# Optimization experiments

Measured on AMD Instinct MI355X. Metric: run time of the kernel, lower is better.

## Reference

```python
import jax, jax.numpy as jnp
import numpy as np

N_GENE, N_DIS = 100_000, 50_000   # node counts per node type
D = 128                            # hidden_channels (= input dim, required by skipsum)
E = 800_000                        # edges per edge type
L = 2                              # num_layers
EPS = 1e-12                        # torch F.normalize eps


def setup_inputs() -> dict:
    key = jax.random.key(0)
    ks = jax.random.split(key, 9)
    s = 1.0 / np.sqrt(D)
    return {
        "x_gene": jax.random.normal(ks[0], (N_GENE, D), jnp.float32),
        "x_disease": jax.random.normal(ks[1], (N_DIS, D), jnp.float32),
        # per (layer, edge_type) SAGEConv weights: lin_l (neighbors), lin_r (root), bias
        # edge_type 0: gene->disease, edge_type 1: disease->gene
        "Wl": jax.random.normal(ks[2], (L, 2, D, D), jnp.float32) * s,
        "Wr": jax.random.normal(ks[3], (L, 2, D, D), jnp.float32) * s,
        "b": jax.random.normal(ks[4], (L, 2, D), jnp.float32) * 0.01,
        "src_g2d": jax.random.randint(ks[5], (E,), 0, N_GENE, dtype=jnp.int32),
        "dst_g2d": jax.random.randint(ks[6], (E,), 0, N_DIS, dtype=jnp.int32),
        "src_d2g": jax.random.randint(ks[7], (E,), 0, N_DIS, dtype=jnp.int32),
        "dst_d2g": jax.random.randint(ks[8], (E,), 0, N_GENE, dtype=jnp.int32),
    }


def _sage(x_src, x_dst, src, dst, Wl, Wr, b, n_dst):
    # SAGEConv with aggr='mean': lin_l(mean_{j in N(i)} x_j) + lin_r(x_i) + bias
    msg = jnp.take(x_src, src, axis=0)                                   # [E, D] gather
    summed = jax.ops.segment_sum(msg, dst, num_segments=n_dst)           # [n_dst, D]
    cnt = jax.ops.segment_sum(jnp.ones_like(src, dtype=x_src.dtype), dst,
                              num_segments=n_dst)                        # [n_dst]
    mean = summed / jnp.maximum(cnt, 1.0)[:, None]                       # isolated nodes -> 0
    return mean @ Wl.T + x_dst @ Wr.T + b


def _l2norm(x):
    n = jnp.linalg.norm(x, axis=-1, keepdims=True)
    return x / jnp.maximum(n, EPS)


def reference(x_gene, x_disease, Wl, Wr, b, src_g2d, dst_g2d, src_d2g, dst_d2g):
    xg, xd = x_gene, x_disease
    for i in range(L):
        # to_hetero: one conv per edge type; macro_aggregation='sum' across edge types
        # (each dst type here receives exactly one edge type)
        hd = _sage(xg, xd, src_g2d, dst_g2d, Wl[i, 0], Wr[i, 0], b[i, 0], N_DIS)
        hg = _sage(xd, xg, src_d2g, dst_d2g, Wl[i, 1], Wr[i, 1], b[i, 1], N_GENE)
        if i < L - 1:  # hidden layers get the activation
            hg, hd = jax.nn.relu(hg), jax.nn.relu(hd)
        # L2_norm=True -> normalize every layer
        hg, hd = _l2norm(hg), _l2norm(hd)
        # skipsum
        xg, xd = hg + xg, hd + xd
    return xg, xd
```

## Files before the change

kernel.cpp:

```cpp
#include <hip/hip_runtime.h>
#include <math.h>

#define NG 100000
#define ND 50000
#define NTOT 150000
#define DIM 128
#define NE 800000
#define EPSN 1e-12f

#define RPB 256
#define NBT_D2 196
#define NBT_G2 391

#define NBK 586
#define SCB 128
#define EPB 12500

typedef __bf16 bf16x8 __attribute__((ext_vector_type(8)));
typedef float f32x4 __attribute__((ext_vector_type(4)));
typedef unsigned int uint32;

__device__ __forceinline__ ushort rne_bf16(float f) {
  uint32 u = __builtin_bit_cast(uint32, f);
  u += 0x7fffu + ((u >> 16) & 1u);
  return (ushort)(u >> 16);
}


__global__ void zero_ints(int* __restrict__ p, int n) {
  int i = blockIdx.x * 256 + threadIdx.x;
  if (i < n) p[i] = 0;
}

__global__ void bucket_count(const int* __restrict__ dst_g2d, const int* __restrict__ dst_d2g,
                             int* __restrict__ bcnt) {
  __shared__ int h[NBK];
  for (int j = threadIdx.x; j < NBK; j += 256) h[j] = 0;
  __syncthreads();
  int stride = gridDim.x * 256;
  for (int i = blockIdx.x * 256 + threadIdx.x; i < 2 * NE; i += stride) {
    int d = (i < NE) ? dst_g2d[i] : ND + dst_d2g[i - NE];
    atomicAdd(&h[d >> 8], 1);
  }
  __syncthreads();
  for (int j = threadIdx.x; j < NBK; j += 256)
    if (h[j]) atomicAdd(&bcnt[j], h[j]);
}

__global__ void bucket_scan(const int* __restrict__ bcnt, int* __restrict__ bbase,
                            int* __restrict__ bcur) {
  __shared__ int s[1024];
  int t = threadIdx.x;
  s[t] = (t < NBK) ? bcnt[t] : 0;
  __syncthreads();
  for (int off = 1; off < 1024; off <<= 1) {
    int v = (t >= off) ? s[t - off] : 0;
    __syncthreads();
    s[t] += v;
    __syncthreads();
  }
  if (t < NBK) {
    int e = (t > 0) ? s[t - 1] : 0;
    bbase[t] = e;
    bcur[t] = e;
  }
  if (t == 0) bbase[NBK] = 2 * NE;
}

__global__ void bucket_scatter(const int* __restrict__ src_g2d, const int* __restrict__ dst_g2d,
                               const int* __restrict__ src_d2g, const int* __restrict__ dst_d2g,
                               int* __restrict__ bcur, int2* __restrict__ pairs) {
  __shared__ int h[NBK];
  __shared__ int base[NBK];
  int e0 = blockIdx.x * EPB;
  int e1 = e0 + EPB;
  if (e1 > 2 * NE) e1 = 2 * NE;
  for (int j = threadIdx.x; j < NBK; j += 256) h[j] = 0;
  __syncthreads();
  for (int i = e0 + threadIdx.x; i < e1; i += 256) {
    int d = (i < NE) ? dst_g2d[i] : ND + dst_d2g[i - NE];
    atomicAdd(&h[d >> 8], 1);
  }
  __syncthreads();
  for (int j = threadIdx.x; j < NBK; j += 256) {
    int c = h[j];
    base[j] = c ? atomicAdd(&bcur[j], c) : 0;
    h[j] = 0;
  }
  __syncthreads();
  for (int i = e0 + threadIdx.x; i < e1; i += 256) {
    int d, s;
    if (i < NE) {
      d = dst_g2d[i];
      s = src_g2d[i];
    } else {
      d = ND + dst_d2g[i - NE];
      s = src_d2g[i - NE];
    }
    int bkt = d >> 8;
    int p = base[bkt] + atomicAdd(&h[bkt], 1);
    pairs[p] = make_int2(d, s);
  }
}

__global__ void bucket_to_csr(const int* __restrict__ bbase, const int2* __restrict__ pairs,
                              int* __restrict__ off, int* __restrict__ csr) {
  __shared__ int cnt[256];
  __shared__ int ss[256];
  int b = blockIdx.x, t = threadIdx.x;
  int n0 = b << 8;
  int s0 = bbase[b], s1 = bbase[b + 1];
  cnt[t] = 0;
  __syncthreads();
  for (int i = s0 + t; i < s1; i += 256) atomicAdd(&cnt[pairs[i].x - n0], 1);
  __syncthreads();
  int x = cnt[t];
  ss[t] = x;
  __syncthreads();
  for (int o = 1; o < 256; o <<= 1) {
    int y = (t >= o) ? ss[t - o] : 0;
    __syncthreads();
    ss[t] += y;
    __syncthreads();
  }
  int abs0 = s0 + ss[t] - x;
  int node = n0 + t;
  if (node < NTOT) off[node] = abs0;
  if (node == NTOT - 1) off[NTOT] = 2 * NE;
  __syncthreads();
  cnt[t] = abs0;
  __syncthreads();
  for (int i = s0 + t; i < s1; i += 256) {
    int2 e = pairs[i];
    int p = atomicAdd(&cnt[e.x - n0], 1);
    csr[p] = e.y;
  }
}


__global__ void to_bf16_all(const float* __restrict__ xg, const float* __restrict__ xd,
                            ushort* __restrict__ yg, ushort* __restrict__ yd) {
  int i = blockIdx.x * 256 + threadIdx.x;
  if (i >= NTOT * 16) return;
  const float* x;
  ushort* y;
  int j;
  if (i < NG * 16) {
    x = xg; y = yg; j = i;
  } else {
    x = xd; y = yd; j = i - NG * 16;
  }
  const float4* px = (const float4*)x;
  float4 a = px[2 * j], b = px[2 * j + 1];
  float v[8] = {a.x, a.y, a.z, a.w, b.x, b.y, b.z, b.w};
  uint32 u[4];
#pragma unroll
  for (int k = 0; k < 4; k++)
    u[k] = (uint32)rne_bf16(v[2 * k]) | ((uint32)rne_bf16(v[2 * k + 1]) << 16);
  ((int4*)y)[j] = make_int4((int)u[0], (int)u[1], (int)u[2], (int)u[3]);
}


__global__ void split_w(const float* __restrict__ Wl, const float* __restrict__ Wr,
                        ushort* __restrict__ WlH, ushort* __restrict__ WlL,
                        ushort* __restrict__ WrH, ushort* __restrict__ WrL) {
  int i = blockIdx.x * 256 + threadIdx.x;
  if (i >= 4 * 128 * 128) return;
  {
    float a = Wl[i];
    uint32 u = __builtin_bit_cast(uint32, a);
    float hf = __builtin_bit_cast(float, u & 0xffff0000u);
    WlH[i] = (ushort)(u >> 16);
    WlL[i] = (ushort)(__builtin_bit_cast(uint32, a - hf) >> 16);
  }
  {
    float a = Wr[i];
    uint32 u = __builtin_bit_cast(uint32, a);
    float hf = __builtin_bit_cast(float, u & 0xffff0000u);
    WrH[i] = (ushort)(u >> 16);
    WrL[i] = (ushort)(__builtin_bit_cast(uint32, a - hf) >> 16);
  }
}


__device__ __forceinline__ void acc8(float* a, int4 u) {
  uint32 w;
  w = (uint32)u.x;
  a[0] += __builtin_bit_cast(float, w << 16);
  a[1] += __builtin_bit_cast(float, w & 0xffff0000u);
  w = (uint32)u.y;
  a[2] += __builtin_bit_cast(float, w << 16);
  a[3] += __builtin_bit_cast(float, w & 0xffff0000u);
  w = (uint32)u.z;
  a[4] += __builtin_bit_cast(float, w << 16);
  a[5] += __builtin_bit_cast(float, w & 0xffff0000u);
  w = (uint32)u.w;
  a[6] += __builtin_bit_cast(float, w << 16);
  a[7] += __builtin_bit_cast(float, w & 0xffff0000u);
}

__global__ void agg_comb(const ushort* __restrict__ xg_bf, const ushort* __restrict__ xd_bf,
                         const int* __restrict__ off, const int* __restrict__ csr,
                         ushort* __restrict__ agg_bf) {
  int node = (blockIdx.x * 256 + threadIdx.x) >> 4;
  if (node >= NTOT) return;
  int l16 = threadIdx.x & 15;
  const int4* xs = (const int4*)((node < ND) ? xg_bf : xd_bf);
  int e0 = off[node], e1 = off[node + 1];
  float a[8] = {0.f, 0.f, 0.f, 0.f, 0.f, 0.f, 0.f, 0.f};
  int e = e0;
  for (; e + 3 < e1; e += 4) {
    int s0 = csr[e], s1 = csr[e + 1], s2 = csr[e + 2], s3 = csr[e + 3];
    int4 v0 = xs[(size_t)s0 * 16 + l16];
    int4 v1 = xs[(size_t)s1 * 16 + l16];
    int4 v2 = xs[(size_t)s2 * 16 + l16];
    int4 v3 = xs[(size_t)s3 * 16 + l16];
    acc8(a, v0);
    acc8(a, v1);
    acc8(a, v2);
    acc8(a, v3);
  }
  for (; e + 1 < e1; e += 2) {
    int s0 = csr[e], s1 = csr[e + 1];
    int4 v0 = xs[(size_t)s0 * 16 + l16];
    int4 v1 = xs[(size_t)s1 * 16 + l16];
    acc8(a, v0);
    acc8(a, v1);
  }
  if (e < e1) acc8(a, xs[(size_t)csr[e] * 16 + l16]);
  int deg = e1 - e0;
  float inv = (deg > 0) ? 1.f / (float)deg : 0.f;
  uint32 u[4];
#pragma unroll
  for (int j = 0; j < 4; j++)
    u[j] = (uint32)rne_bf16(a[2 * j] * inv) | ((uint32)rne_bf16(a[2 * j + 1] * inv) << 16);
  *(int4*)&agg_bf[(size_t)node * DIM + l16 * 8] =
      make_int4((int)u[0], (int)u[1], (int)u[2], (int)u[3]);
}


__device__ __forceinline__ void split8(const float* xp, bf16x8& hi, bf16x8& lo) {
  float4 f0 = *(const float4*)xp;
  float4 f1 = *(const float4*)(xp + 4);
  float v[8] = {f0.x, f0.y, f0.z, f0.w, f1.x, f1.y, f1.z, f1.w};
  uint32 hw[4], lw[4];
#pragma unroll
  for (int j = 0; j < 4; j++) {
    uint32 u0 = __builtin_bit_cast(uint32, v[2 * j]);
    uint32 u1 = __builtin_bit_cast(uint32, v[2 * j + 1]);
    float hf0 = __builtin_bit_cast(float, u0 & 0xffff0000u);
    float hf1 = __builtin_bit_cast(float, u1 & 0xffff0000u);
    uint32 l0 = __builtin_bit_cast(uint32, v[2 * j] - hf0) >> 16;
    uint32 l1 = __builtin_bit_cast(uint32, v[2 * j + 1] - hf1) >> 16;
    hw[j] = (u0 >> 16) | ((u1 >> 16) << 16);
    lw[j] = l0 | (l1 << 16);
  }
  hi = __builtin_bit_cast(bf16x8, make_int4((int)hw[0], (int)hw[1], (int)hw[2], (int)hw[3]));
  lo = __builtin_bit_cast(bf16x8, make_int4((int)lw[0], (int)lw[1], (int)lw[2], (int)lw[3]));
}

__launch_bounds__(256, 2)
__global__ void sage_dual(const ushort* __restrict__ agg_bf, const float* __restrict__ xd,
                          const float* __restrict__ xg, const ushort* __restrict__ WlH,
                          const ushort* __restrict__ WlL, const ushort* __restrict__ WrH,
                          const ushort* __restrict__ WrL, const float* __restrict__ bias_all,
                          float* __restrict__ outd, float* __restrict__ outg,
                          ushort* __restrict__ xbf_d, ushort* __restrict__ xbf_g, int layer,
                          int relu, int write_bf) {
  __shared__ __align__(16) char smem[65536];

  int b = blockIdx.x;
  const float* X;
  float* O;
  ushort* OBF;
  int n, set, r0g, cbase;
  if (b < NBT_D2) {
    X = xd; O = outd; OBF = xbf_d; n = ND; set = layer * 2; r0g = b * RPB; cbase = 0;
  } else {
    X = xg; O = outg; OBF = xbf_g; n = NG; set = layer * 2 + 1;
    r0g = (b - NBT_D2) * RPB; cbase = ND;
  }
  const ushort* Wplanes[4] = {WlH + set * 16384, WlL + set * 16384, WrH + set * 16384,
                              WrL + set * 16384};
  const float* bias = bias_all + set * 128;

  int tid = threadIdx.x;
  int wave = tid >> 6, lane = tid & 63;
  int m = lane & 15, q = lane >> 4;

  auto stageW = [&](const ushort* Ph, const ushort* Pl) {
#pragma unroll
    for (int i = 0; i < 16; i++) {
      int c = tid + i * 256;
      int p = c >> 11;
      int Bl = (c & 2047) * 16;
      const ushort* src = p ? Pl : Ph;
      int4 v = *(const int4*)((const char*)src + Bl);
      int dst = p * 32768 + (Bl ^ (((Bl >> 8) & 7) << 4));
      *(int4*)(smem + dst) = v;
    }
  };

  f32x4 acc[4][8];
#pragma unroll
  for (int mt = 0; mt < 4; mt++)
#pragma unroll
    for (int nt = 0; nt < 8; nt++) acc[mt][nt] = (f32x4)0.f;

  int rb = r0g + wave * 64;

  stageW(Wplanes[0], Wplanes[1]);
  __syncthreads();
#pragma unroll
  for (int ks = 0; ks < 4; ks++) {
    int kc = ks * 32 + q * 8;
    int kb = ks * 64 + q * 16;
    bf16x8 a[4];
#pragma unroll
    for (int mt = 0; mt < 4; mt++) {
      int r = rb + mt * 16 + m;
      if (r >= n) r = n - 1;
      a[mt] = __builtin_bit_cast(bf16x8, *(const int4*)&agg_bf[(size_t)(cbase + r) * DIM + kc]);
    }
#pragma unroll
    for (int nt = 0; nt < 8; nt++) {
      int nn = nt * 16 + m;
      int wb = (nn * 256 + kb) ^ ((nn & 7) << 4);
      bf16x8 bh = *(const bf16x8*)(smem + wb);
      bf16x8 bl = *(const bf16x8*)(smem + 32768 + wb);
#pragma unroll
      for (int mt = 0; mt < 4; mt++) {
        acc[mt][nt] = __builtin_amdgcn_mfma_f32_16x16x32_bf16(a[mt], bh, acc[mt][nt], 0, 0, 0);
        acc[mt][nt] = __builtin_amdgcn_mfma_f32_16x16x32_bf16(a[mt], bl, acc[mt][nt], 0, 0, 0);
      }
    }
  }
  __syncthreads();

  stageW(Wplanes[2], Wplanes[3]);
  __syncthreads();
#pragma unroll
  for (int ks = 0; ks < 4; ks++) {
    int kc = ks * 32 + q * 8;
    int kb = ks * 64 + q * 16;
    bf16x8 ah[4], al[4];
#pragma unroll
    for (int mt = 0; mt < 4; mt++) {
      int r = rb + mt * 16 + m;
      if (r >= n) r = n - 1;
      split8(&X[(size_t)r * DIM + kc], ah[mt], al[mt]);
    }
#pragma unroll
    for (int nt = 0; nt < 8; nt++) {
      int nn = nt * 16 + m;
      int wb = (nn * 256 + kb) ^ ((nn & 7) << 4);
      bf16x8 bh = *(const bf16x8*)(smem + wb);
      bf16x8 bl = *(const bf16x8*)(smem + 32768 + wb);
#pragma unroll
      for (int mt = 0; mt < 4; mt++) {
        acc[mt][nt] = __builtin_amdgcn_mfma_f32_16x16x32_bf16(ah[mt], bh, acc[mt][nt], 0, 0, 0);
        acc[mt][nt] = __builtin_amdgcn_mfma_f32_16x16x32_bf16(ah[mt], bl, acc[mt][nt], 0, 0, 0);
        acc[mt][nt] = __builtin_amdgcn_mfma_f32_16x16x32_bf16(al[mt], bh, acc[mt][nt], 0, 0, 0);
      }
    }
  }
  __syncthreads();

  float bb[8];
#pragma unroll
  for (int nt = 0; nt < 8; nt++) bb[nt] = bias[nt * 16 + m];

  const int S = 132;
  float* wbuf = (float*)smem + wave * (16 * S);

  int half = lane >> 5;
  int c4 = (lane & 31) * 4;

#pragma unroll
  for (int mt = 0; mt < 4; mt++) {
#pragma unroll
    for (int reg = 0; reg < 4; reg++) {
      float h[8];
      float ss = 0.f;
#pragma unroll
      for (int nt = 0; nt < 8; nt++) {
        float v = acc[mt][nt][reg] + bb[nt];
        if (relu) v = fmaxf(v, 0.f);
        h[nt] = v;
        ss += v * v;
      }
      ss += __shfl_xor(ss, 1);
      ss += __shfl_xor(ss, 2);
      ss += __shfl_xor(ss, 4);
      ss += __shfl_xor(ss, 8);
      float inv = 1.f / fmaxf(sqrtf(ss), EPSN);
      int rrel = q * 4 + reg;
#pragma unroll
      for (int nt = 0; nt < 8; nt++) wbuf[rrel * S + nt * 16 + m] = h[nt] * inv;
    }
#pragma unroll
    for (int i = 0; i < 8; i++) {
      int rrel = i * 2 + half;
      int R = rb + mt * 16 + rrel;
      if (R < n) {
        f32x4 hv = *(const f32x4*)&wbuf[rrel * S + c4];
        float4 xr = *(const float4*)&X[(size_t)R * DIM + c4];
        float4 o;
        o.x = hv[0] + xr.x;
        o.y = hv[1] + xr.y;
        o.z = hv[2] + xr.z;
        o.w = hv[3] + xr.w;
        *(float4*)&O[(size_t)R * DIM + c4] = o;
        if (write_bf) {
          int2 pk = make_int2((int)((uint32)rne_bf16(o.x) | ((uint32)rne_bf16(o.y) << 16)),
                              (int)((uint32)rne_bf16(o.z) | ((uint32)rne_bf16(o.w) << 16)));
          *(int2*)&OBF[(size_t)R * DIM + c4] = pk;
        }
      }
    }
  }
}


extern "C" void kernel_launch(void* const* d_in, const int* in_sizes, int n_in,
                              void* d_out, int out_size, void* d_ws, size_t ws_size,
                              hipStream_t stream) {
  const float* xg0 = (const float*)d_in[0];
  const float* xd0 = (const float*)d_in[1];
  const float* Wl = (const float*)d_in[2];
  const float* Wr = (const float*)d_in[3];
  const float* bs = (const float*)d_in[4];
  const int* src_g2d = (const int*)d_in[5];
  const int* dst_g2d = (const int*)d_in[6];
  const int* src_d2g = (const int*)d_in[7];
  const int* dst_d2g = (const int*)d_in[8];

  float* out_xg = (float*)d_out;
  float* out_xd = (float*)d_out + (size_t)NG * DIM;

  char* p = (char*)d_ws;
  auto alloc = [&](size_t bytes) -> char* {
    char* q = p;
    p += (bytes + 255) & ~(size_t)255;
    return q;
  };
  int* off = (int*)alloc((NTOT + 1) * 4);
  int* csr = (int*)alloc((size_t)2 * NE * 4);
  int* bcnt = (int*)alloc(NBK * 4);
  int* bbase = (int*)alloc((NBK + 1) * 4);
  int* bcur = (int*)alloc(NBK * 4);
  char* big = alloc((size_t)NTOT * DIM * 2);
  int2* pairs = (int2*)big;
  ushort* agg_bf = (ushort*)big;
  ushort* xg_bf = (ushort*)alloc((size_t)NG * DIM * 2);
  ushort* xd_bf = (ushort*)alloc((size_t)ND * DIM * 2);
  ushort* WlH = (ushort*)alloc((size_t)4 * 128 * 128 * 2);
  ushort* WlL = (ushort*)alloc((size_t)4 * 128 * 128 * 2);
  ushort* WrH = (ushort*)alloc((size_t)4 * 128 * 128 * 2);
  ushort* WrL = (ushort*)alloc((size_t)4 * 128 * 128 * 2);

  const int TB = 256;

  split_w<<<256, TB, 0, stream>>>(Wl, Wr, WlH, WlL, WrH, WrL);
  to_bf16_all<<<(NTOT * 16 + TB - 1) / TB, TB, 0, stream>>>(xg0, xd0, xg_bf, xd_bf);

  zero_ints<<<(NBK + TB - 1) / TB, TB, 0, stream>>>(bcnt, NBK);
  bucket_count<<<256, TB, 0, stream>>>(dst_g2d, dst_d2g, bcnt);
  bucket_scan<<<1, 1024, 0, stream>>>(bcnt, bbase, bcur);
  bucket_scatter<<<SCB, TB, 0, stream>>>(src_g2d, dst_g2d, src_d2g, dst_d2g, bcur, pairs);
  bucket_to_csr<<<NBK, TB, 0, stream>>>(bbase, pairs, off, csr);

  int aggBlocks = (NTOT * 16 + TB - 1) / TB;
  int sageBlocks = NBT_D2 + NBT_G2;

  agg_comb<<<aggBlocks, TB, 0, stream>>>(xg_bf, xd_bf, off, csr, agg_bf);
  sage_dual<<<sageBlocks, TB, 0, stream>>>(agg_bf, xd0, xg0, WlH, WlL, WrH, WrL, bs, out_xd,
                                           out_xg, xd_bf, xg_bf, 0, 1, 1);

  agg_comb<<<aggBlocks, TB, 0, stream>>>(xg_bf, xd_bf, off, csr, agg_bf);
  sage_dual<<<sageBlocks, TB, 0, stream>>>(agg_bf, out_xd, out_xg, WlH, WlL, WrH, WrL, bs,
                                           out_xd, out_xg, xd_bf, xg_bf, 1, 0, 0);
}
```

Before: 483.6 us.

## Prefetch aggregated and root activations into registers to overlap loads with MFMA

The dense GEMM kernel now loads all agg_bf A-fragments for every k-step up front, before staging the first weight planes. The Wr planes are loaded into registers before the barrier, so global latency overlaps the first GEMM's tail. The x root rows for the next k-step are software-prefetched while the current step's MFMAs run. The cost is much higher register pressure (aV, xV and wv arrays) under launch_bounds(256,2), which risks spills or lower occupancy.

Result: slower. 533.0 us (+10.2%).

```diff
diff --git a/kernel.cpp b/kernel.cpp
--- a/kernel.cpp
+++ b/kernel.cpp
@@ -239,9 +239,7 @@
 }
 
 
-__device__ __forceinline__ void split8(const float* xp, bf16x8& hi, bf16x8& lo) {
-  float4 f0 = *(const float4*)xp;
-  float4 f1 = *(const float4*)(xp + 4);
+__device__ __forceinline__ void split8v(float4 f0, float4 f1, bf16x8& hi, bf16x8& lo) {
   float v[8] = {f0.x, f0.y, f0.z, f0.w, f1.x, f1.y, f1.z, f1.w};
   uint32 hw[4], lw[4];
 #pragma unroll
@@ -287,19 +285,35 @@
   int tid = threadIdx.x;
   int wave = tid >> 6, lane = tid & 63;
   int m = lane & 15, q = lane >> 4;
-
-  auto stageW = [&](const ushort* Ph, const ushort* Pl) {
+  int rb = r0g + wave * 64;
+
+  int rp[4];
+#pragma unroll
+  for (int mt = 0; mt < 4; mt++) {
+    int r = rb + mt * 16 + m;
+    rp[mt] = (r >= n) ? (n - 1) : r;
+  }
+
+  int4 aV[4][4];
+#pragma unroll
+  for (int ks = 0; ks < 4; ks++)
+#pragma unroll
+    for (int mt = 0; mt < 4; mt++)
+      aV[ks][mt] = *(const int4*)&agg_bf[(size_t)(cbase + rp[mt]) * DIM + ks * 32 + q * 8];
+
+  {
 #pragma unroll
     for (int i = 0; i < 16; i++) {
       int c = tid + i * 256;
       int p = c >> 11;
       int Bl = (c & 2047) * 16;
-      const ushort* src = p ? Pl : Ph;
+      const ushort* src = p ? Wplanes[1] : Wplanes[0];
       int4 v = *(const int4*)((const char*)src + Bl);
       int dst = p * 32768 + (Bl ^ (((Bl >> 8) & 7) << 4));
       *(int4*)(smem + dst) = v;
     }
-  };
+  }
+  __syncthreads();
 
   f32x4 acc[4][8];
 #pragma unroll
@@ -307,21 +321,9 @@
 #pragma unroll
     for (int nt = 0; nt < 8; nt++) acc[mt][nt] = (f32x4)0.f;
 
-  int rb = r0g + wave * 64;
-
-  stageW(Wplanes[0], Wplanes[1]);
-  __syncthreads();
 #pragma unroll
   for (int ks = 0; ks < 4; ks++) {
-    int kc = ks * 32 + q * 8;
     int kb = ks * 64 + q * 16;
-    bf16x8 a[4];
-#pragma unroll
-    for (int mt = 0; mt < 4; mt++) {
-      int r = rb + mt * 16 + m;
-      if (r >= n) r = n - 1;
-      a[mt] = __builtin_bit_cast(bf16x8, *(const int4*)&agg_bf[(size_t)(cbase + r) * DIM + kc]);
-    }
 #pragma unroll
     for (int nt = 0; nt < 8; nt++) {
       int nn = nt * 16 + m;
@@ -330,25 +332,53 @@
       bf16x8 bl = *(const bf16x8*)(smem + 32768 + wb);
 #pragma unroll
       for (int mt = 0; mt < 4; mt++) {
-        acc[mt][nt] = __builtin_amdgcn_mfma_f32_16x16x32_bf16(a[mt], bh, acc[mt][nt], 0, 0, 0);
-        acc[mt][nt] = __builtin_amdgcn_mfma_f32_16x16x32_bf16(a[mt], bl, acc[mt][nt], 0, 0, 0);
+        bf16x8 a = __builtin_bit_cast(bf16x8, aV[ks][mt]);
+        acc[mt][nt] = __builtin_amdgcn_mfma_f32_16x16x32_bf16(a, bh, acc[mt][nt], 0, 0, 0);
+        acc[mt][nt] = __builtin_amdgcn_mfma_f32_16x16x32_bf16(a, bl, acc[mt][nt], 0, 0, 0);
       }
     }
   }
-  __syncthreads();
-
-  stageW(Wplanes[2], Wplanes[3]);
-  __syncthreads();
+
+  float4 xV[4][2];
+#pragma unroll
+  for (int mt = 0; mt < 4; mt++) {
+#pragma unroll
+    for (int h = 0; h < 2; h++)
+      xV[mt][h] = *(const float4*)&X[(size_t)rp[mt] * DIM + q * 8 + h * 4];
+  }
+  int4 wv[16];
+#pragma unroll
+  for (int i = 0; i < 16; i++) {
+    int c = tid + i * 256;
+    int p = c >> 11;
+    int Bl = (c & 2047) * 16;
+    const ushort* src = p ? Wplanes[3] : Wplanes[2];
+    wv[i] = *(const int4*)((const char*)src + Bl);
+  }
+  __syncthreads();
+#pragma unroll
+  for (int i = 0; i < 16; i++) {
+    int c = tid + i * 256;
+    int p = c >> 11;
+    int Bl = (c & 2047) * 16;
+    int dst = p * 32768 + (Bl ^ (((Bl >> 8) & 7) << 4));
+    *(int4*)(smem + dst) = wv[i];
+  }
+  __syncthreads();
+
 #pragma unroll
   for (int ks = 0; ks < 4; ks++) {
-    int kc = ks * 32 + q * 8;
     int kb = ks * 64 + q * 16;
     bf16x8 ah[4], al[4];
 #pragma unroll
-    for (int mt = 0; mt < 4; mt++) {
-      int r = rb + mt * 16 + m;
-      if (r >= n) r = n - 1;
-      split8(&X[(size_t)r * DIM + kc], ah[mt], al[mt]);
+    for (int mt = 0; mt < 4; mt++) split8v(xV[mt][0], xV[mt][1], ah[mt], al[mt]);
+    if (ks < 3) {
+#pragma unroll
+      for (int mt = 0; mt < 4; mt++) {
+#pragma unroll
+        for (int h = 0; h < 2; h++)
+          xV[mt][h] = *(const float4*)&X[(size_t)rp[mt] * DIM + (ks + 1) * 32 + q * 8 + h * 4];
+      }
     }
 #pragma unroll
     for (int nt = 0; nt < 8; nt++) {
```
